# Optimization experiments

Measured on AMD Instinct MI355X. Metric: run time of the kernel, lower is better.

The kernel has to match this reference:

```python
import jax, jax.numpy as jnp
import numpy as np

N_NODES = 50000
N_EDGES = 800000
IN_DIM = 128
HID_DIM = 128


def setup_inputs() -> dict:
    key = jax.random.key(0)
    k1, k2, k3, k4 = jax.random.split(key, 4)
    x = jax.random.normal(k1, (N_NODES, IN_DIM), dtype=jnp.float32)
    src = jax.random.randint(k2, (N_EDGES,), 0, N_NODES, dtype=jnp.int64)
    dst = jax.random.randint(k3, (N_EDGES,), 0, N_NODES, dtype=jnp.int64)
    W = jax.random.normal(k4, (IN_DIM, HID_DIM), dtype=jnp.float32) * (1.0 / np.sqrt(IN_DIM))
    b = jnp.zeros((HID_DIM,), dtype=jnp.float32)
    return {"x": x, "src": src, "dst": dst, "W": W, "b": b}


def reference(x, src, dst, W, b):
    # DGL GraphConv, norm='both': out = D_in^{-1/2} A D_out^{-1/2} x W + b
    n = x.shape[0]
    ones = jnp.ones((src.shape[0],), dtype=x.dtype)
    deg_out = jax.ops.segment_sum(ones, src, num_segments=n)  # out-degree of src side
    deg_in = jax.ops.segment_sum(ones, dst, num_segments=n)   # in-degree of dst side
    norm_src = jnp.clip(deg_out, 1.0, None) ** -0.5           # [N]
    norm_dst = jnp.clip(deg_in, 1.0, None) ** -0.5            # [N]
    h = x * norm_src[:, None]                                 # [N, in_dim]
    agg = jax.ops.segment_sum(h[src], dst, num_segments=n)    # SpMM: sum messages at dst
    agg = agg * norm_dst[:, None]
    return agg @ W + b
```

## Files before the change

kernel.cpp:

```cpp
#include <hip/hip_runtime.h>
#include <hip/hip_bf16.h>

#define DIM   128
#define BM    64
#define HALF_NODES 25088
#define HALF_PAIRS (HALF_NODES / 2)
#define FULL_PAIRS (2 * HALF_PAIRS)

typedef short  bf16x8 __attribute__((ext_vector_type(8)));
typedef float  f32x4  __attribute__((ext_vector_type(4)));

__device__ __forceinline__ ushort f2bf(float f) {
    uint u = __float_as_uint(f);
    return (ushort)((u + 0x7FFFu + ((u >> 16) & 1u)) >> 16);
}

__global__ __launch_bounds__(1024) void hist_kernel(const int* __restrict__ src,
                                                    const int* __restrict__ dst,
                                                    uint* __restrict__ histD,
                                                    uint* __restrict__ histS,
                                                    int* __restrict__ rank,
                                                    int n_edges, int pairs_row,
                                                    int nhalves, int chunk,
                                                    int nblkD) {
    __shared__ uint h[FULL_PAIRS];
    const int  tid  = threadIdx.x;
    const bool isD  = (int)blockIdx.x < nblkD;
    const int  c    = isD ? (int)blockIdx.x : (int)blockIdx.x - nblkD;
    const int  beg  = c * chunk;
    const int  end  = min(beg + chunk, n_edges);
    const int* key  = isD ? dst : src;
    uint*      outb = isD ? histD : histS;

    for (int hbase = 0; hbase < nhalves; hbase += 2) {
        const int plo    = hbase * HALF_PAIRS;
        const int wpairs = min(FULL_PAIRS, pairs_row - plo);
        const int wnodes = wpairs * 2;
        const int lo     = plo * 2;
        for (int j = tid; j < wpairs; j += 1024) h[j] = 0;
        __syncthreads();
        for (int e = beg + tid; e < end; e += 1024) {
            int r = key[e] - lo;
            if ((unsigned)r < (unsigned)wnodes) {
                uint old = atomicAdd(&h[r >> 1], 1u << ((r & 1) * 16));
                if (isD)
                    rank[e] = (r & 1) ? (int)(old >> 16) : (int)(old & 0xFFFFu);
            }
        }
        __syncthreads();
        uint* row = outb + (size_t)c * pairs_row + plo;
        for (int j = tid; j < wpairs; j += 1024) row[j] = h[j];
        __syncthreads();
    }
}

__global__ __launch_bounds__(256) void prefix_kernel(uint* __restrict__ histD,
                                                     const uint* __restrict__ histS,
                                                     int* __restrict__ deg_in,
                                                     float* __restrict__ norm_src,
                                                     const float* __restrict__ W,
                                                     ushort* __restrict__ WT,
                                                     int pairs_row, int n_nodes,
                                                     int nchunk, int nblk_main) {
    if ((int)blockIdx.x >= nblk_main) {
        int idx = ((int)blockIdx.x - nblk_main) * 256 + threadIdx.x;
        if (idx < DIM * DIM) {
            int k = idx >> 7, c = idx & 127;
            WT[c * DIM + k] = f2bf(W[idx]);
        }
        return;
    }
    int id = blockIdx.x * 256 + threadIdx.x;
    bool isS = id >= pairs_row;
    int j = isS ? id - pairs_row : id;
    if (j >= pairs_row) return;
    if (isS) {
        const uint* col = histS + j;
        uint run0 = 0, run1 = 0;
        for (int c = 0; c < nchunk; ++c) {
            uint v = col[(size_t)c * pairs_row];
            run0 += v & 0xFFFFu;
            run1 += v >> 16;
        }
        int n0 = 2 * j, n1 = 2 * j + 1;
        if (n0 < n_nodes) norm_src[n0] = rsqrtf(fmaxf((float)run0, 1.0f));
        if (n1 < n_nodes) norm_src[n1] = rsqrtf(fmaxf((float)run1, 1.0f));
    } else {
        uint* col = histD + j;
        uint run0 = 0, run1 = 0;
        for (int c = 0; c < nchunk; ++c) {
            uint v = col[(size_t)c * pairs_row];
            col[(size_t)c * pairs_row] = run0 | (run1 << 16);
            run0 += v & 0xFFFFu;
            run1 += v >> 16;
        }
        deg_in[2 * j]     = (int)run0;
        deg_in[2 * j + 1] = (int)run1;
    }
}

__global__ __launch_bounds__(1024) void scan4_kernel(const int* __restrict__ deg,
                                                     int* __restrict__ offs, int n) {
    __shared__ int w1[16], w2[16];
    const int tid = threadIdx.x, lane = tid & 63, wid = tid >> 6;
    const int base = blockIdx.x * 4096;

    int part = 0;
    for (int i = base ? tid : n; i < base; i += 1024) part += deg[i];
#pragma unroll
    for (int o = 32; o; o >>= 1) part += __shfl_xor(part, o);
    if (lane == 0) w1[wid] = part;
    __syncthreads();
    int prefix = 0;
#pragma unroll
    for (int k = 0; k < 16; ++k) prefix += w1[k];

    int i0 = base + tid * 4;
    int e0 = (i0 + 0 < n) ? deg[i0 + 0] : 0;
    int e1 = (i0 + 1 < n) ? deg[i0 + 1] : 0;
    int e2 = (i0 + 2 < n) ? deg[i0 + 2] : 0;
    int e3 = (i0 + 3 < n) ? deg[i0 + 3] : 0;
    int s  = e0 + e1 + e2 + e3;
    int sc = s;
#pragma unroll
    for (int o = 1; o < 64; o <<= 1) {
        int t = __shfl_up(sc, o);
        if (lane >= o) sc += t;
    }
    if (lane == 63) w2[wid] = sc;
    __syncthreads();
    int wpre = 0;
    for (int k = 0; k < wid; ++k) wpre += w2[k];
    int excl = prefix + wpre + sc - s;
    int o1 = excl + e0, o2 = o1 + e1, o3 = o2 + e2, o4 = o3 + e3;
    if (i0 + 0 < n) offs[i0 + 1] = o1;
    if (i0 + 1 < n) offs[i0 + 2] = o2;
    if (i0 + 2 < n) offs[i0 + 3] = o3;
    if (i0 + 3 < n) offs[i0 + 4] = o4;
    if (base == 0 && tid == 0) offs[0] = 0;
}

__global__ __launch_bounds__(256) void fill_kernel(const int* __restrict__ src,
                                                   const int* __restrict__ dst,
                                                   const int* __restrict__ offs,
                                                   const uint* __restrict__ histD,
                                                   const int* __restrict__ rank,
                                                   int* __restrict__ esrc,
                                                   int n_edges, int pairs_row,
                                                   int chunk) {
    int e = blockIdx.x * 256 + threadIdx.x;
    if (e >= n_edges) return;
    int t = dst[e];
    int c = e / chunk;
    uint pf = histD[(size_t)c * pairs_row + (t >> 1)];
    int pref = (t & 1) ? (int)(pf >> 16) : (int)(pf & 0xFFFFu);
    esrc[offs[t] + pref + rank[e]] = src[e];
}

__global__ __launch_bounds__(256, 4) void gemmx_kernel(const float* __restrict__ x,
                                                       const ushort* __restrict__ WT,
                                                       const float* __restrict__ norm_src,
                                                       ushort* __restrict__ h,
                                                       int n_nodes) {
    __shared__ ushort WsT[DIM * DIM];
    const int tid = threadIdx.x;

    {
        const uint4* wsrc = reinterpret_cast<const uint4*>(WT);
#pragma unroll
        for (int i = 0; i < 8; ++i) {
            int linear = tid + i * 256;
            uint4 v = wsrc[linear];
            int byte = linear * 16;
            int c = byte >> 8;
            int swz = byte ^ ((c & 7) << 4);
            *reinterpret_cast<uint4*>(reinterpret_cast<char*>(WsT) + swz) = v;
        }
    }
    __syncthreads();

    const int lane = tid & 63;
    const int w    = tid >> 6;
    const int r0   = blockIdx.x * BM;
    const int rowm = r0 + w * 16 + (lane & 15);
    const int rowc = min(rowm, n_nodes - 1);
    const float4* X4 = reinterpret_cast<const float4*>(x);

    f32x4 acc[8];
#pragma unroll
    for (int t = 0; t < 8; ++t) acc[t] = (f32x4){0.f, 0.f, 0.f, 0.f};

#pragma unroll
    for (int s = 0; s < 4; ++s) {
        int idx = rowc * 32 + s * 8 + (lane >> 4) * 2;
        float4 v0 = X4[idx];
        float4 v1 = X4[idx + 1];
        bf16x8 a;
        a[0] = (short)f2bf(v0.x); a[1] = (short)f2bf(v0.y);
        a[2] = (short)f2bf(v0.z); a[3] = (short)f2bf(v0.w);
        a[4] = (short)f2bf(v1.x); a[5] = (short)f2bf(v1.y);
        a[6] = (short)f2bf(v1.z); a[7] = (short)f2bf(v1.w);
#pragma unroll
        for (int t = 0; t < 8; ++t) {
            int c   = t * 16 + (lane & 15);
            int ofs = c * 256 + s * 64 + (lane >> 4) * 16;
            ofs ^= (c & 7) << 4;
            bf16x8 b = *reinterpret_cast<const bf16x8*>(
                reinterpret_cast<const char*>(WsT) + ofs);
            acc[t] = __builtin_amdgcn_mfma_f32_16x16x32_bf16(a, b, acc[t], 0, 0, 0);
        }
    }

#pragma unroll
    for (int i = 0; i < 4; ++i) {
        int row = r0 + w * 16 + (lane >> 4) * 4 + i;
        if (row < n_nodes) {
            float ns = norm_src[row];
            ushort* hp = h + (size_t)row * DIM + (lane & 15);
#pragma unroll
            for (int t = 0; t < 8; ++t)
                hp[t * 16] = f2bf(acc[t][i] * ns);
        }
    }
}

__global__ __launch_bounds__(256) void gather_kernel(const ushort* __restrict__ h,
                                                     const int* __restrict__ esrc,
                                                     const int* __restrict__ offs,
                                                     const float* __restrict__ bg,
                                                     float* __restrict__ out,
                                                     int n_nodes) {
    int node = blockIdx.x * 4 + (threadIdx.x >> 6);
    if (node >= n_nodes) return;
    int lane = threadIdx.x & 63;
    int j = offs[node], end = offs[node + 1];
    int deg = end - j;
    const uint* hp = reinterpret_cast<const uint*>(h);
    float ax[8], ay[8];
#pragma unroll
    for (int q = 0; q < 8; ++q) { ax[q] = 0.f; ay[q] = 0.f; }
    for (; j + 7 < end; j += 8) {
        int   si[8];
        uint  u[8];
#pragma unroll
        for (int q = 0; q < 8; ++q) si[q] = esrc[j + q];
#pragma unroll
        for (int q = 0; q < 8; ++q) u[q] = hp[(size_t)si[q] * 64 + lane];
#pragma unroll
        for (int q = 0; q < 8; ++q) {
            ax[q] += __uint_as_float(u[q] << 16);
            ay[q] += __uint_as_float(u[q] & 0xFFFF0000u);
        }
    }
    for (; j + 3 < end; j += 4) {
        int  si[4];
        uint u[4];
#pragma unroll
        for (int q = 0; q < 4; ++q) si[q] = esrc[j + q];
#pragma unroll
        for (int q = 0; q < 4; ++q) u[q] = hp[(size_t)si[q] * 64 + lane];
#pragma unroll
        for (int q = 0; q < 4; ++q) {
            ax[q] += __uint_as_float(u[q] << 16);
            ay[q] += __uint_as_float(u[q] & 0xFFFF0000u);
        }
    }
    for (; j < end; ++j) {
        uint u = hp[(size_t)esrc[j] * 64 + lane];
        ax[0] += __uint_as_float(u << 16);
        ay[0] += __uint_as_float(u & 0xFFFF0000u);
    }
    float sx = ((ax[0] + ax[1]) + (ax[2] + ax[3])) + ((ax[4] + ax[5]) + (ax[6] + ax[7]));
    float sy = ((ay[0] + ay[1]) + (ay[2] + ay[3])) + ((ay[4] + ay[5]) + (ay[6] + ay[7]));
    float nd = rsqrtf(fmaxf((float)deg, 1.0f));
    float2 bv = reinterpret_cast<const float2*>(bg)[lane];
    float2 r;
    r.x = sx * nd + bv.x;
    r.y = sy * nd + bv.y;
    reinterpret_cast<float2*>(out)[(size_t)node * 64 + lane] = r;
}

extern "C" void kernel_launch(void* const* d_in, const int* in_sizes, int n_in,
                              void* d_out, int out_size, void* d_ws, size_t ws_size,
                              hipStream_t stream) {
    const float* x   = (const float*)d_in[0];
    const int*   src = (const int*)d_in[1];
    const int*   dst = (const int*)d_in[2];
    const float* W   = (const float*)d_in[3];
    const float* b   = (const float*)d_in[4];
    float* out = (float*)d_out;

    const int n_nodes = in_sizes[0] / DIM;
    const int n_edges = in_sizes[1];

    const int nhalves   = (n_nodes + HALF_NODES - 1) / HALF_NODES;
    const int npad      = nhalves * HALF_NODES;
    const int pairs_row = npad / 2;

    auto need = [&](int C) -> size_t {
        return 2ull * n_nodes * DIM + 2ull * DIM * DIM +
               4ull * ((size_t)2 * npad + 1 + n_nodes +
                       2ull * C * pairs_row + 2ull * n_edges);
    };
    int C = 64;
    if (ws_size < need(64)) C = 32;
    if (ws_size < need(32)) C = 16;
    const int chunk = (n_edges + C - 1) / C;

    ushort* h        = (ushort*)d_ws;
    ushort* WT       = h + (size_t)n_nodes * DIM;
    int*    deg_in   = (int*)(WT + DIM * DIM);
    int*    offs     = deg_in + npad;
    float*  norm_src = (float*)(offs + npad + 1);
    uint*   histD    = (uint*)(norm_src + n_nodes);
    uint*   histS    = histD + (size_t)C * pairs_row;
    int*    rank     = (int*)(histS + (size_t)C * pairs_row);
    int*    esrc     = rank + n_edges;

    const int egrid    = (n_edges + 255) / 256;
    const int nblkpref = (2 * pairs_row + 255) / 256;

    hist_kernel<<<2 * C, 1024, 0, stream>>>(src, dst, histD, histS, rank,
                                            n_edges, pairs_row, nhalves, chunk, C);
    prefix_kernel<<<nblkpref + (DIM * DIM + 255) / 256, 256, 0, stream>>>(
        histD, histS, deg_in, norm_src, W, WT, pairs_row, n_nodes, C, nblkpref);
    gemmx_kernel<<<(n_nodes + BM - 1) / BM, 256, 0, stream>>>(
        x, WT, norm_src, h, n_nodes);
    scan4_kernel<<<(npad + 4095) / 4096, 1024, 0, stream>>>(deg_in, offs, npad);
    fill_kernel<<<egrid, 256, 0, stream>>>(src, dst, offs, histD, rank, esrc,
                                           n_edges, pairs_row, chunk);
    gather_kernel<<<(n_nodes + 3) / 4, 256, 0, stream>>>(
        h, esrc, offs, b, out, n_nodes);
}
```

Measured before the change: 106.9 us.

## Fuse degree scan into GEMM launch, vectorize fill, persistent-wave gather

Folds the offsets scan into the gemmx launch as extra blocks, so one kernel launch and its serialization gap go away. The fill kernel now handles two edges per thread with int2 loads. The gather kernel becomes a grid-stride persistent kernel with 1024-thread blocks on a fixed grid of 512. The trade-off is that the scan blocks now use 256 threads over 1024 elements each, so there are more of them and each redoes its prefix sum from the start. The persistent gather may also balance load worse across waves.

```diff
diff --git a/kernel.cpp b/kernel.cpp
--- a/kernel.cpp
+++ b/kernel.cpp
@@ -99,71 +99,56 @@
     }
 }
 
-__global__ __launch_bounds__(1024) void scan4_kernel(const int* __restrict__ deg,
-                                                     int* __restrict__ offs, int n) {
-    __shared__ int w1[16], w2[16];
-    const int tid = threadIdx.x, lane = tid & 63, wid = tid >> 6;
-    const int base = blockIdx.x * 4096;
-
-    int part = 0;
-    for (int i = base ? tid : n; i < base; i += 1024) part += deg[i];
-#pragma unroll
-    for (int o = 32; o; o >>= 1) part += __shfl_xor(part, o);
-    if (lane == 0) w1[wid] = part;
-    __syncthreads();
-    int prefix = 0;
-#pragma unroll
-    for (int k = 0; k < 16; ++k) prefix += w1[k];
-
-    int i0 = base + tid * 4;
-    int e0 = (i0 + 0 < n) ? deg[i0 + 0] : 0;
-    int e1 = (i0 + 1 < n) ? deg[i0 + 1] : 0;
-    int e2 = (i0 + 2 < n) ? deg[i0 + 2] : 0;
-    int e3 = (i0 + 3 < n) ? deg[i0 + 3] : 0;
-    int s  = e0 + e1 + e2 + e3;
-    int sc = s;
-#pragma unroll
-    for (int o = 1; o < 64; o <<= 1) {
-        int t = __shfl_up(sc, o);
-        if (lane >= o) sc += t;
-    }
-    if (lane == 63) w2[wid] = sc;
-    __syncthreads();
-    int wpre = 0;
-    for (int k = 0; k < wid; ++k) wpre += w2[k];
-    int excl = prefix + wpre + sc - s;
-    int o1 = excl + e0, o2 = o1 + e1, o3 = o2 + e2, o4 = o3 + e3;
-    if (i0 + 0 < n) offs[i0 + 1] = o1;
-    if (i0 + 1 < n) offs[i0 + 2] = o2;
-    if (i0 + 2 < n) offs[i0 + 3] = o3;
-    if (i0 + 3 < n) offs[i0 + 4] = o4;
-    if (base == 0 && tid == 0) offs[0] = 0;
-}
-
-__global__ __launch_bounds__(256) void fill_kernel(const int* __restrict__ src,
-                                                   const int* __restrict__ dst,
-                                                   const int* __restrict__ offs,
-                                                   const uint* __restrict__ histD,
-                                                   const int* __restrict__ rank,
-                                                   int* __restrict__ esrc,
-                                                   int n_edges, int pairs_row,
-                                                   int chunk) {
-    int e = blockIdx.x * 256 + threadIdx.x;
-    if (e >= n_edges) return;
-    int t = dst[e];
-    int c = e / chunk;
-    uint pf = histD[(size_t)c * pairs_row + (t >> 1)];
-    int pref = (t & 1) ? (int)(pf >> 16) : (int)(pf & 0xFFFFu);
-    esrc[offs[t] + pref + rank[e]] = src[e];
-}
-
 __global__ __launch_bounds__(256, 4) void gemmx_kernel(const float* __restrict__ x,
                                                        const ushort* __restrict__ WT,
                                                        const float* __restrict__ norm_src,
                                                        ushort* __restrict__ h,
-                                                       int n_nodes) {
+                                                       const int* __restrict__ deg,
+                                                       int* __restrict__ offs,
+                                                       int n_nodes, int nscan,
+                                                       int ngemm) {
     __shared__ ushort WsT[DIM * DIM];
     const int tid = threadIdx.x;
+
+    if ((int)blockIdx.x >= ngemm) {
+        __shared__ int w1[4], w2[4];
+        const int lane = tid & 63, wid = tid >> 6;
+        const int base = ((int)blockIdx.x - ngemm) * 1024;
+        const int n    = nscan;
+
+        int part = 0;
+        for (int i = base ? tid : n; i < base; i += 256) part += deg[i];
+#pragma unroll
+        for (int o = 32; o; o >>= 1) part += __shfl_xor(part, o);
+        if (lane == 0) w1[wid] = part;
+        __syncthreads();
+        int prefix = w1[0] + w1[1] + w1[2] + w1[3];
+
+        int i0 = base + tid * 4;
+        int e0 = (i0 + 0 < n) ? deg[i0 + 0] : 0;
+        int e1 = (i0 + 1 < n) ? deg[i0 + 1] : 0;
+        int e2 = (i0 + 2 < n) ? deg[i0 + 2] : 0;
+        int e3 = (i0 + 3 < n) ? deg[i0 + 3] : 0;
+        int s  = e0 + e1 + e2 + e3;
+        int sc = s;
+#pragma unroll
+        for (int o = 1; o < 64; o <<= 1) {
+            int t = __shfl_up(sc, o);
+            if (lane >= o) sc += t;
+        }
+        if (lane == 63) w2[wid] = sc;
+        __syncthreads();
+        int wpre = 0;
+        for (int k = 0; k < wid; ++k) wpre += w2[k];
+        int excl = prefix + wpre + sc - s;
+        int o1 = excl + e0, o2 = o1 + e1, o3 = o2 + e2, o4 = o3 + e3;
+        if (i0 + 0 < n) offs[i0 + 1] = o1;
+        if (i0 + 1 < n) offs[i0 + 2] = o2;
+        if (i0 + 2 < n) offs[i0 + 3] = o3;
+        if (i0 + 3 < n) offs[i0 + 4] = o4;
+        if (base == 0 && tid == 0) offs[0] = 0;
+        return;
+    }
 
     {
         const uint4* wsrc = reinterpret_cast<const uint4*>(WT);
@@ -224,60 +209,93 @@
     }
 }
 
-__global__ __launch_bounds__(256) void gather_kernel(const ushort* __restrict__ h,
-                                                     const int* __restrict__ esrc,
-                                                     const int* __restrict__ offs,
-                                                     const float* __restrict__ bg,
-                                                     float* __restrict__ out,
-                                                     int n_nodes) {
-    int node = blockIdx.x * 4 + (threadIdx.x >> 6);
-    if (node >= n_nodes) return;
-    int lane = threadIdx.x & 63;
-    int j = offs[node], end = offs[node + 1];
-    int deg = end - j;
-    const uint* hp = reinterpret_cast<const uint*>(h);
-    float ax[8], ay[8];
-#pragma unroll
-    for (int q = 0; q < 8; ++q) { ax[q] = 0.f; ay[q] = 0.f; }
-    for (; j + 7 < end; j += 8) {
-        int   si[8];
-        uint  u[8];
-#pragma unroll
-        for (int q = 0; q < 8; ++q) si[q] = esrc[j + q];
-#pragma unroll
-        for (int q = 0; q < 8; ++q) u[q] = hp[(size_t)si[q] * 64 + lane];
-#pragma unroll
-        for (int q = 0; q < 8; ++q) {
-            ax[q] += __uint_as_float(u[q] << 16);
-            ay[q] += __uint_as_float(u[q] & 0xFFFF0000u);
-        }
-    }
-    for (; j + 3 < end; j += 4) {
-        int  si[4];
-        uint u[4];
-#pragma unroll
-        for (int q = 0; q < 4; ++q) si[q] = esrc[j + q];
-#pragma unroll
-        for (int q = 0; q < 4; ++q) u[q] = hp[(size_t)si[q] * 64 + lane];
-#pragma unroll
-        for (int q = 0; q < 4; ++q) {
-            ax[q] += __uint_as_float(u[q] << 16);
-            ay[q] += __uint_as_float(u[q] & 0xFFFF0000u);
-        }
-    }
-    for (; j < end; ++j) {
-        uint u = hp[(size_t)esrc[j] * 64 + lane];
-        ax[0] += __uint_as_float(u << 16);
-        ay[0] += __uint_as_float(u & 0xFFFF0000u);
-    }
-    float sx = ((ax[0] + ax[1]) + (ax[2] + ax[3])) + ((ax[4] + ax[5]) + (ax[6] + ax[7]));
-    float sy = ((ay[0] + ay[1]) + (ay[2] + ay[3])) + ((ay[4] + ay[5]) + (ay[6] + ay[7]));
-    float nd = rsqrtf(fmaxf((float)deg, 1.0f));
+__global__ __launch_bounds__(256) void fill_kernel(const int* __restrict__ src,
+                                                   const int* __restrict__ dst,
+                                                   const int* __restrict__ offs,
+                                                   const uint* __restrict__ histD,
+                                                   const int* __restrict__ rank,
+                                                   int* __restrict__ esrc,
+                                                   int n_edges, int pairs_row,
+                                                   int chunk) {
+    int e0 = (blockIdx.x * 256 + threadIdx.x) * 2;
+    if (e0 >= n_edges) return;
+    if (e0 + 1 < n_edges) {
+        int2 t2 = *reinterpret_cast<const int2*>(dst + e0);
+        int2 s2 = *reinterpret_cast<const int2*>(src + e0);
+        int2 r2 = *reinterpret_cast<const int2*>(rank + e0);
+        int  c0 = e0 / chunk, c1 = (e0 + 1) / chunk;
+        uint pf0 = histD[(size_t)c0 * pairs_row + (t2.x >> 1)];
+        uint pf1 = histD[(size_t)c1 * pairs_row + (t2.y >> 1)];
+        int p0 = (t2.x & 1) ? (int)(pf0 >> 16) : (int)(pf0 & 0xFFFFu);
+        int p1 = (t2.y & 1) ? (int)(pf1 >> 16) : (int)(pf1 & 0xFFFFu);
+        esrc[offs[t2.x] + p0 + r2.x] = s2.x;
+        esrc[offs[t2.y] + p1 + r2.y] = s2.y;
+    } else {
+        int t = dst[e0];
+        int c = e0 / chunk;
+        uint pf = histD[(size_t)c * pairs_row + (t >> 1)];
+        int pref = (t & 1) ? (int)(pf >> 16) : (int)(pf & 0xFFFFu);
+        esrc[offs[t] + pref + rank[e0]] = src[e0];
+    }
+}
+
+__global__ __launch_bounds__(1024) void gather_kernel(const ushort* __restrict__ h,
+                                                      const int* __restrict__ esrc,
+                                                      const int* __restrict__ offs,
+                                                      const float* __restrict__ bg,
+                                                      float* __restrict__ out,
+                                                      int n_nodes) {
+    const int lane   = threadIdx.x & 63;
+    const int wid    = blockIdx.x * 16 + (threadIdx.x >> 6);
+    const int nwaves = gridDim.x * 16;
+    const uint* hp   = reinterpret_cast<const uint*>(h);
     float2 bv = reinterpret_cast<const float2*>(bg)[lane];
-    float2 r;
-    r.x = sx * nd + bv.x;
-    r.y = sy * nd + bv.y;
-    reinterpret_cast<float2*>(out)[(size_t)node * 64 + lane] = r;
+
+    for (int node = wid; node < n_nodes; node += nwaves) {
+        int j = offs[node], end = offs[node + 1];
+        int deg = end - j;
+        float ax[8], ay[8];
+#pragma unroll
+        for (int q = 0; q < 8; ++q) { ax[q] = 0.f; ay[q] = 0.f; }
+        for (; j + 7 < end; j += 8) {
+            int  si[8];
+            uint u[8];
+#pragma unroll
+            for (int q = 0; q < 8; ++q) si[q] = esrc[j + q];
+#pragma unroll
+            for (int q = 0; q < 8; ++q) u[q] = hp[(size_t)si[q] * 64 + lane];
+#pragma unroll
+            for (int q = 0; q < 8; ++q) {
+                ax[q] += __uint_as_float(u[q] << 16);
+                ay[q] += __uint_as_float(u[q] & 0xFFFF0000u);
+            }
+        }
+        for (; j + 3 < end; j += 4) {
+            int  si[4];
+            uint u[4];
+#pragma unroll
+            for (int q = 0; q < 4; ++q) si[q] = esrc[j + q];
+#pragma unroll
+            for (int q = 0; q < 4; ++q) u[q] = hp[(size_t)si[q] * 64 + lane];
+#pragma unroll
+            for (int q = 0; q < 4; ++q) {
+                ax[q] += __uint_as_float(u[q] << 16);
+                ay[q] += __uint_as_float(u[q] & 0xFFFF0000u);
+            }
+        }
+        for (; j < end; ++j) {
+            uint u = hp[(size_t)esrc[j] * 64 + lane];
+            ax[0] += __uint_as_float(u << 16);
+            ay[0] += __uint_as_float(u & 0xFFFF0000u);
+        }
+        float sx = ((ax[0] + ax[1]) + (ax[2] + ax[3])) + ((ax[4] + ax[5]) + (ax[6] + ax[7]));
+        float sy = ((ay[0] + ay[1]) + (ay[2] + ay[3])) + ((ay[4] + ay[5]) + (ay[6] + ay[7]));
+        float nd = rsqrtf(fmaxf((float)deg, 1.0f));
+        float2 r;
+        r.x = sx * nd + bv.x;
+        r.y = sy * nd + bv.y;
+        reinterpret_cast<float2*>(out)[(size_t)node * 64 + lane] = r;
+    }
 }
 
 extern "C" void kernel_launch(void* const* d_in, const int* in_sizes, int n_in,
@@ -317,18 +335,17 @@
     int*    rank     = (int*)(histS + (size_t)C * pairs_row);
     int*    esrc     = rank + n_edges;
 
-    const int egrid    = (n_edges + 255) / 256;
     const int nblkpref = (2 * pairs_row + 255) / 256;
+    const int ngemm    = (n_nodes + BM - 1) / BM;
+    const int nscanblk = (npad + 1023) / 1024;
 
     hist_kernel<<<2 * C, 1024, 0, stream>>>(src, dst, histD, histS, rank,
                                             n_edges, pairs_row, nhalves, chunk, C);
     prefix_kernel<<<nblkpref + (DIM * DIM + 255) / 256, 256, 0, stream>>>(
         histD, histS, deg_in, norm_src, W, WT, pairs_row, n_nodes, C, nblkpref);
-    gemmx_kernel<<<(n_nodes + BM - 1) / BM, 256, 0, stream>>>(
-        x, WT, norm_src, h, n_nodes);
-    scan4_kernel<<<(npad + 4095) / 4096, 1024, 0, stream>>>(deg_in, offs, npad);
-    fill_kernel<<<egrid, 256, 0, stream>>>(src, dst, offs, histD, rank, esrc,
-                                           n_edges, pairs_row, chunk);
-    gather_kernel<<<(n_nodes + 3) / 4, 256, 0, stream>>>(
-        h, esrc, offs, b, out, n_nodes);
-}
+    gemmx_kernel<<<ngemm + nscanblk, 256, 0, stream>>>(
+        x, WT, norm_src, h, deg_in, offs, n_nodes, npad, ngemm);
+    fill_kernel<<<(n_edges / 2 + 255) / 256, 256, 0, stream>>>(
+        src, dst, offs, histD, rank, esrc, n_edges, pairs_row, chunk);
+    gather_kernel<<<512, 1024, 0, stream>>>(h, esrc, offs, b, out, n_nodes);
+}
```

Result: slower. 117.3 us (+9.7%).

## Fuse histogram, prefix, scan and fill into one cooperative kernel

Applied to the files above, without the earlier changes.

Replaces the four separate preprocessing launches (histogram, column prefix, degree scan, CSR fill) with one cooperative kernel that uses grid-wide syncs between phases. The histogram now uses a single 25088-node LDS window per pass (half the previous shared array), so more blocks can be resident, and loops over windows instead of covering two halves at once. The aim is to remove kernel launch gaps and tail effects between the small preprocessing stages. In exchange it pays for grid.sync barriers, runs with a grid sized by occupancy, and does twice as many histogram passes over the edge chunks.

```diff
diff --git a/kernel.cpp b/kernel.cpp
--- a/kernel.cpp
+++ b/kernel.cpp
@@ -1,11 +1,13 @@
 #include <hip/hip_runtime.h>
 #include <hip/hip_bf16.h>
+#include <hip/hip_cooperative_groups.h>
+
+namespace cg = cooperative_groups;
 
 #define DIM   128
 #define BM    64
-#define HALF_NODES 25088
-#define HALF_PAIRS (HALF_NODES / 2)
-#define FULL_PAIRS (2 * HALF_PAIRS)
+#define WIN_NODES 25088
+#define WIN_PAIRS (WIN_NODES / 2)
 
 typedef short  bf16x8 __attribute__((ext_vector_type(8)));
 typedef float  f32x4  __attribute__((ext_vector_type(4)));
@@ -15,146 +17,135 @@
     return (ushort)((u + 0x7FFFu + ((u >> 16) & 1u)) >> 16);
 }
 
-__global__ __launch_bounds__(1024) void hist_kernel(const int* __restrict__ src,
-                                                    const int* __restrict__ dst,
-                                                    uint* __restrict__ histD,
-                                                    uint* __restrict__ histS,
-                                                    int* __restrict__ rank,
-                                                    int n_edges, int pairs_row,
-                                                    int nhalves, int chunk,
-                                                    int nblkD) {
-    __shared__ uint h[FULL_PAIRS];
-    const int  tid  = threadIdx.x;
-    const bool isD  = (int)blockIdx.x < nblkD;
-    const int  c    = isD ? (int)blockIdx.x : (int)blockIdx.x - nblkD;
-    const int  beg  = c * chunk;
-    const int  end  = min(beg + chunk, n_edges);
-    const int* key  = isD ? dst : src;
-    uint*      outb = isD ? histD : histS;
-
-    for (int hbase = 0; hbase < nhalves; hbase += 2) {
-        const int plo    = hbase * HALF_PAIRS;
-        const int wpairs = min(FULL_PAIRS, pairs_row - plo);
-        const int wnodes = wpairs * 2;
-        const int lo     = plo * 2;
-        for (int j = tid; j < wpairs; j += 1024) h[j] = 0;
+__global__ __launch_bounds__(1024, 8) void preproc_kernel(
+    const int* __restrict__ src, const int* __restrict__ dst,
+    uint* __restrict__ histD, uint* __restrict__ histS,
+    int* __restrict__ rank, int* __restrict__ deg_in, int* __restrict__ offs,
+    float* __restrict__ norm_src, const float* __restrict__ W,
+    ushort* __restrict__ WT, int* __restrict__ esrc,
+    int n_edges, int n_nodes, int pairs_row, int nwin, int chunk, int C) {
+    cg::grid_group grid = cg::this_grid();
+    __shared__ uint hh[WIN_PAIRS];
+    __shared__ int  w1[16], w2[16];
+    const int tid = threadIdx.x;
+    const int b   = blockIdx.x;
+    const int npad = 2 * pairs_row;
+
+    for (int blk = b; blk < 2 * C; blk += gridDim.x) {
+        const bool isD = blk < C;
+        const int  c   = isD ? blk : blk - C;
+        const int  beg = c * chunk;
+        const int  end = min(beg + chunk, n_edges);
+        const int* key = isD ? dst : src;
+        uint* outb     = isD ? histD : histS;
+        for (int half = 0; half < nwin; ++half) {
+            const int plo    = half * WIN_PAIRS;
+            const int wpairs = min(WIN_PAIRS, pairs_row - plo);
+            const int wnodes = wpairs * 2;
+            const int lo     = plo * 2;
+            for (int j = tid; j < wpairs; j += 1024) hh[j] = 0;
+            __syncthreads();
+            for (int e = beg + tid; e < end; e += 1024) {
+                int r = key[e] - lo;
+                if ((unsigned)r < (unsigned)wnodes) {
+                    uint old = atomicAdd(&hh[r >> 1], 1u << ((r & 1) * 16));
+                    if (isD)
+                        rank[e] = (r & 1) ? (int)(old >> 16) : (int)(old & 0xFFFFu);
+                }
+            }
+            __syncthreads();
+            uint* row = outb + (size_t)c * pairs_row + plo;
+            for (int j = tid; j < wpairs; j += 1024) row[j] = hh[j];
+            __syncthreads();
+        }
+    }
+    grid.sync();
+
+    {
+        const int total = 2 * pairs_row + DIM * DIM;
+        const int stride = gridDim.x * 1024;
+        for (int id = b * 1024 + tid; id < total; id += stride) {
+            if (id < pairs_row) {
+                uint* col = histD + id;
+                uint run0 = 0, run1 = 0;
+                for (int c = 0; c < C; ++c) {
+                    uint v = col[(size_t)c * pairs_row];
+                    col[(size_t)c * pairs_row] = run0 | (run1 << 16);
+                    run0 += v & 0xFFFFu;
+                    run1 += v >> 16;
+                }
+                deg_in[2 * id]     = (int)run0;
+                deg_in[2 * id + 1] = (int)run1;
+            } else if (id < 2 * pairs_row) {
+                int j = id - pairs_row;
+                const uint* col = histS + j;
+                uint run0 = 0, run1 = 0;
+                for (int c = 0; c < C; ++c) {
+                    uint v = col[(size_t)c * pairs_row];
+                    run0 += v & 0xFFFFu;
+                    run1 += v >> 16;
+                }
+                int n0 = 2 * j, n1 = 2 * j + 1;
+                if (n0 < n_nodes) norm_src[n0] = rsqrtf(fmaxf((float)run0, 1.0f));
+                if (n1 < n_nodes) norm_src[n1] = rsqrtf(fmaxf((float)run1, 1.0f));
+            } else {
+                int idx = id - 2 * pairs_row;
+                int k = idx >> 7, cc = idx & 127;
+                WT[cc * DIM + k] = f2bf(W[idx]);
+            }
+        }
+    }
+    grid.sync();
+
+    for (int base = b * 4096; base < npad; base += gridDim.x * 4096) {
+        const int lane = tid & 63, wid = tid >> 6;
+        const int n = npad;
+        int part = 0;
+        for (int i = base ? tid : n; i < base; i += 1024) part += deg_in[i];
+#pragma unroll
+        for (int o = 32; o; o >>= 1) part += __shfl_xor(part, o);
+        if (lane == 0) w1[wid] = part;
         __syncthreads();
-        for (int e = beg + tid; e < end; e += 1024) {
-            int r = key[e] - lo;
-            if ((unsigned)r < (unsigned)wnodes) {
-                uint old = atomicAdd(&h[r >> 1], 1u << ((r & 1) * 16));
-                if (isD)
-                    rank[e] = (r & 1) ? (int)(old >> 16) : (int)(old & 0xFFFFu);
-            }
-        }
+        int prefix = 0;
+#pragma unroll
+        for (int k = 0; k < 16; ++k) prefix += w1[k];
+
+        int i0 = base + tid * 4;
+        int e0 = (i0 + 0 < n) ? deg_in[i0 + 0] : 0;
+        int e1 = (i0 + 1 < n) ? deg_in[i0 + 1] : 0;
+        int e2 = (i0 + 2 < n) ? deg_in[i0 + 2] : 0;
+        int e3 = (i0 + 3 < n) ? deg_in[i0 + 3] : 0;
+        int s  = e0 + e1 + e2 + e3;
+        int sc = s;
+#pragma unroll
+        for (int o = 1; o < 64; o <<= 1) {
+            int t = __shfl_up(sc, o);
+            if (lane >= o) sc += t;
+        }
+        if (lane == 63) w2[wid] = sc;
         __syncthreads();
-        uint* row = outb + (size_t)c * pairs_row + plo;
-        for (int j = tid; j < wpairs; j += 1024) row[j] = h[j];
-        __syncthreads();
-    }
-}
-
-__global__ __launch_bounds__(256) void prefix_kernel(uint* __restrict__ histD,
-                                                     const uint* __restrict__ histS,
-                                                     int* __restrict__ deg_in,
-                                                     float* __restrict__ norm_src,
-                                                     const float* __restrict__ W,
-                                                     ushort* __restrict__ WT,
-                                                     int pairs_row, int n_nodes,
-                                                     int nchunk, int nblk_main) {
-    if ((int)blockIdx.x >= nblk_main) {
-        int idx = ((int)blockIdx.x - nblk_main) * 256 + threadIdx.x;
-        if (idx < DIM * DIM) {
-            int k = idx >> 7, c = idx & 127;
-            WT[c * DIM + k] = f2bf(W[idx]);
-        }
-        return;
-    }
-    int id = blockIdx.x * 256 + threadIdx.x;
-    bool isS = id >= pairs_row;
-    int j = isS ? id - pairs_row : id;
-    if (j >= pairs_row) return;
-    if (isS) {
-        const uint* col = histS + j;
-        uint run0 = 0, run1 = 0;
-        for (int c = 0; c < nchunk; ++c) {
-            uint v = col[(size_t)c * pairs_row];
-            run0 += v & 0xFFFFu;
-            run1 += v >> 16;
-        }
-        int n0 = 2 * j, n1 = 2 * j + 1;
-        if (n0 < n_nodes) norm_src[n0] = rsqrtf(fmaxf((float)run0, 1.0f));
-        if (n1 < n_nodes) norm_src[n1] = rsqrtf(fmaxf((float)run1, 1.0f));
-    } else {
-        uint* col = histD + j;
-        uint run0 = 0, run1 = 0;
-        for (int c = 0; c < nchunk; ++c) {
-            uint v = col[(size_t)c * pairs_row];
-            col[(size_t)c * pairs_row] = run0 | (run1 << 16);
-            run0 += v & 0xFFFFu;
-            run1 += v >> 16;
-        }
-        deg_in[2 * j]     = (int)run0;
-        deg_in[2 * j + 1] = (int)run1;
-    }
-}
-
-__global__ __launch_bounds__(1024) void scan4_kernel(const int* __restrict__ deg,
-                                                     int* __restrict__ offs, int n) {
-    __shared__ int w1[16], w2[16];
-    const int tid = threadIdx.x, lane = tid & 63, wid = tid >> 6;
-    const int base = blockIdx.x * 4096;
-
-    int part = 0;
-    for (int i = base ? tid : n; i < base; i += 1024) part += deg[i];
-#pragma unroll
-    for (int o = 32; o; o >>= 1) part += __shfl_xor(part, o);
-    if (lane == 0) w1[wid] = part;
-    __syncthreads();
-    int prefix = 0;
-#pragma unroll
-    for (int k = 0; k < 16; ++k) prefix += w1[k];
-
-    int i0 = base + tid * 4;
-    int e0 = (i0 + 0 < n) ? deg[i0 + 0] : 0;
-    int e1 = (i0 + 1 < n) ? deg[i0 + 1] : 0;
-    int e2 = (i0 + 2 < n) ? deg[i0 + 2] : 0;
-    int e3 = (i0 + 3 < n) ? deg[i0 + 3] : 0;
-    int s  = e0 + e1 + e2 + e3;
-    int sc = s;
-#pragma unroll
-    for (int o = 1; o < 64; o <<= 1) {
-        int t = __shfl_up(sc, o);
-        if (lane >= o) sc += t;
-    }
-    if (lane == 63) w2[wid] = sc;
-    __syncthreads();
-    int wpre = 0;
-    for (int k = 0; k < wid; ++k) wpre += w2[k];
-    int excl = prefix + wpre + sc - s;
-    int o1 = excl + e0, o2 = o1 + e1, o3 = o2 + e2, o4 = o3 + e3;
-    if (i0 + 0 < n) offs[i0 + 1] = o1;
-    if (i0 + 1 < n) offs[i0 + 2] = o2;
-    if (i0 + 2 < n) offs[i0 + 3] = o3;
-    if (i0 + 3 < n) offs[i0 + 4] = o4;
-    if (base == 0 && tid == 0) offs[0] = 0;
-}
-
-__global__ __launch_bounds__(256) void fill_kernel(const int* __restrict__ src,
-                                                   const int* __restrict__ dst,
-                                                   const int* __restrict__ offs,
-                                                   const uint* __restrict__ histD,
-                                                   const int* __restrict__ rank,
-                                                   int* __restrict__ esrc,
-                                                   int n_edges, int pairs_row,
-                                                   int chunk) {
-    int e = blockIdx.x * 256 + threadIdx.x;
-    if (e >= n_edges) return;
-    int t = dst[e];
-    int c = e / chunk;
-    uint pf = histD[(size_t)c * pairs_row + (t >> 1)];
-    int pref = (t & 1) ? (int)(pf >> 16) : (int)(pf & 0xFFFFu);
-    esrc[offs[t] + pref + rank[e]] = src[e];
+        int wpre = 0;
+        for (int k = 0; k < wid; ++k) wpre += w2[k];
+        int excl = prefix + wpre + sc - s;
+        int o1 = excl + e0, o2 = o1 + e1, o3 = o2 + e2, o4 = o3 + e3;
+        if (i0 + 0 < n) offs[i0 + 1] = o1;
+        if (i0 + 1 < n) offs[i0 + 2] = o2;
+        if (i0 + 2 < n) offs[i0 + 3] = o3;
+        if (i0 + 3 < n) offs[i0 + 4] = o4;
+        if (base == 0 && tid == 0) offs[0] = 0;
+    }
+    grid.sync();
+
+    {
+        const int stride = gridDim.x * 1024;
+        for (int e = b * 1024 + tid; e < n_edges; e += stride) {
+            int t = dst[e];
+            int c = e / chunk;
+            uint pf = histD[(size_t)c * pairs_row + (t >> 1)];
+            int pref = (t & 1) ? (int)(pf >> 16) : (int)(pf & 0xFFFFu);
+            esrc[offs[t] + pref + rank[e]] = src[e];
+        }
+    }
 }
 
 __global__ __launch_bounds__(256, 4) void gemmx_kernel(const float* __restrict__ x,
@@ -205,9 +196,9 @@
             int c   = t * 16 + (lane & 15);
             int ofs = c * 256 + s * 64 + (lane >> 4) * 16;
             ofs ^= (c & 7) << 4;
-            bf16x8 b = *reinterpret_cast<const bf16x8*>(
+            bf16x8 bfr = *reinterpret_cast<const bf16x8*>(
                 reinterpret_cast<const char*>(WsT) + ofs);
-            acc[t] = __builtin_amdgcn_mfma_f32_16x16x32_bf16(a, b, acc[t], 0, 0, 0);
+            acc[t] = __builtin_amdgcn_mfma_f32_16x16x32_bf16(a, bfr, acc[t], 0, 0, 0);
         }
     }
 
@@ -293,8 +284,8 @@
     const int n_nodes = in_sizes[0] / DIM;
     const int n_edges = in_sizes[1];
 
-    const int nhalves   = (n_nodes + HALF_NODES - 1) / HALF_NODES;
-    const int npad      = nhalves * HALF_NODES;
+    const int nwin      = (n_nodes + WIN_NODES - 1) / WIN_NODES;
+    const int npad      = nwin * WIN_NODES;
     const int pairs_row = npad / 2;
 
     auto need = [&](int C) -> size_t {
@@ -317,18 +308,32 @@
     int*    rank     = (int*)(histS + (size_t)C * pairs_row);
     int*    esrc     = rank + n_edges;
 
-    const int egrid    = (n_edges + 255) / 256;
-    const int nblkpref = (2 * pairs_row + 255) / 256;
-
-    hist_kernel<<<2 * C, 1024, 0, stream>>>(src, dst, histD, histS, rank,
-                                            n_edges, pairs_row, nhalves, chunk, C);
-    prefix_kernel<<<nblkpref + (DIM * DIM + 255) / 256, 256, 0, stream>>>(
-        histD, histS, deg_in, norm_src, W, WT, pairs_row, n_nodes, C, nblkpref);
+    int occ = 0;
+    hipOccupancyMaxActiveBlocksPerMultiprocessor(&occ, preproc_kernel, 1024, 0);
+    if (occ < 1) occ = 1;
+    int CB = occ * 256;
+    if (CB > 512) CB = 512;
+
+    int ne = n_edges, nn = n_nodes, pr = pairs_row, nw = nwin, ch = chunk, cc = C;
+    void* kargs[] = {
+        (void*)&x
+    };
+    void* args[17];
+    args[0]  = (void*)&src;      args[1]  = (void*)&dst;
+    args[2]  = (void*)&histD;    args[3]  = (void*)&histS;
+    args[4]  = (void*)&rank;     args[5]  = (void*)&deg_in;
+    args[6]  = (void*)&offs;     args[7]  = (void*)&norm_src;
+    args[8]  = (void*)&W;        args[9]  = (void*)&WT;
+    args[10] = (void*)&esrc;     args[11] = (void*)&ne;
+    args[12] = (void*)&nn;       args[13] = (void*)&pr;
+    args[14] = (void*)&nw;       args[15] = (void*)&ch;
+    args[16] = (void*)&cc;
+    (void)kargs;
+
+    hipLaunchCooperativeKernel((const void*)preproc_kernel, dim3(CB), dim3(1024),
+                               args, 0, stream);
     gemmx_kernel<<<(n_nodes + BM - 1) / BM, 256, 0, stream>>>(
         x, WT, norm_src, h, n_nodes);
-    scan4_kernel<<<(npad + 4095) / 4096, 1024, 0, stream>>>(deg_in, offs, npad);
-    fill_kernel<<<egrid, 256, 0, stream>>>(src, dst, offs, histD, rank, esrc,
-                                           n_edges, pairs_row, chunk);
     gather_kernel<<<(n_nodes + 3) / 4, 256, 0, stream>>>(
         h, esrc, offs, b, out, n_nodes);
 }
```

Result: slower. 203.0 us (+89.9%).
